# Kernel optimization log

Hardware: AMD Instinct MI355X
Metric: run time of the kernel (lower is better)

The kernel has to match this reference:

```python
import jax, jax.numpy as jnp
import numpy as np

B, C, T = 2048, 8, 1024
EPS = 1e-5
SLOPE = 1.0 / 128.0


def leaky(x):
    # F.leaky_relu(x, 1/128)
    return jnp.where(x >= 0, x, SLOPE * x)


def batchnorm(h, g, b):
    # training-mode BatchNorm1d over [B, C, T]: stats over (batch, time), biased var
    m = h.mean(axis=(0, 2), keepdims=True)
    v = jnp.mean((h - m) ** 2, axis=(0, 2), keepdims=True)
    return (h - m) * jax.lax.rsqrt(v + EPS) * g[None, :, None] + b[None, :, None]


def setup_inputs() -> dict:
    key = jax.random.key(0)
    ks = jax.random.split(key, 8)
    x = jax.random.normal(ks[0], (B, C, T), dtype=jnp.float32)
    # reservoir pushforward: low-bit random matrix scaled to spectral radius 0.1
    A_raw = jax.random.normal(ks[1], (C, C), dtype=jnp.float32)
    rho = jnp.max(jnp.abs(np.linalg.eigvals(np.asarray(A_raw))))
    A = (0.1 * A_raw / rho).astype(jnp.float32)
    w1 = jax.random.normal(ks[2], (24, 8), dtype=jnp.float32) * (1.0 / np.sqrt(8))
    b1 = jax.random.normal(ks[3], (24,), dtype=jnp.float32) * 0.01
    w2 = jax.random.normal(ks[4], (16, 24), dtype=jnp.float32) * (1.0 / np.sqrt(24))
    b2 = jax.random.normal(ks[5], (16,), dtype=jnp.float32) * 0.01
    w3 = jax.random.normal(ks[6], (11, 48), dtype=jnp.float32) * (1.0 / np.sqrt(48))
    b3 = jax.random.normal(ks[7], (11,), dtype=jnp.float32) * 0.01
    return {
        "x": x, "A": A,
        "bn1_g": jnp.ones((8,), jnp.float32), "bn1_b": jnp.zeros((8,), jnp.float32),
        "w1": w1, "b1": b1, "w2": w2, "b2": b2, "w3": w3, "b3": b3,
        "bn2_g": jnp.ones((11,), jnp.float32), "bn2_b": jnp.zeros((11,), jnp.float32),
    }


def reference(x, A, bn1_g, bn1_b, w1, b1, w2, b2, w3, b3, bn2_g, bn2_b):
    bw = batchnorm(x, bn1_g, bn1_b)  # [B,8,T]

    # --- FSDDRC reservoir: 1024-step sequential recurrence on 8-dim state ---
    xs = jnp.transpose(bw, (2, 0, 1))  # [T,B,8]

    def step(f, xt):
        # nonlin(A @ f + x_t) with nonlin(z) = clamp(4z, -1, 1)
        f_new = jnp.clip(4.0 * (f @ A.T + xt), -1.0, 1.0)
        return f_new, jnp.concatenate([f_new, leaky(f_new)], axis=-1)  # [B,16]

    f0 = jnp.zeros_like(xs[0])
    _, outs = jax.lax.scan(step, f0, xs)  # [T,B,16]
    nl_tdyn = jnp.transpose(outs, (1, 2, 0))  # [B,16,T]

    # --- feedforward branch (mtmt = linear over channel dim) ---
    h = leaky(jnp.einsum("bct,oc->bot", bw, w1) + b1[None, :, None])  # [B,24,T]
    ff = leaky(jnp.einsum("bct,oc->bot", h, w2) + b2[None, :, None])  # [B,16,T]

    stacked = jnp.concatenate([x, bw, ff, nl_tdyn], axis=1)  # [B,48,T]
    pre = jnp.einsum("bct,oc->bot", stacked, w3) + b3[None, :, None]  # [B,11,T]
    assimilated = leaky(batchnorm(pre, bn2_g, bn2_b))
    return assimilated.mean(axis=-1)  # [B,11]
```

## Files before the change

### kernel.cpp

```cpp
#include <hip/hip_runtime.h>
#include <hip/hip_fp16.h>

#define NB 2048
#define NC 8
#define NT 1024
#define EPS 1e-5f
#define SLOPE (1.0f/128.0f)
#define NELEM (2048.0f*1024.0f)
#define TB (NT*NB)

#define PAR_OFF 9216
#define BN2_OFF 1024
#define P2_OFF  10240
#define PF_S4  0
#define PF_O4  8
#define PF_B1F 16
#define PF_B2F 40
#define PF_B3F 56
#define PU_A4   96
#define XT_BYTE  65536
#define PWS_BYTE (65536 + 2048*1024*8*2)

#define ROWH 40
#define ZH   18

typedef _Float16 h2 __attribute__((ext_vector_type(2)));
typedef _Float16 half8 __attribute__((ext_vector_type(8)));
typedef float f32x4 __attribute__((ext_vector_type(4)));
typedef __fp16  fp16v2 __attribute__((ext_vector_type(2)));
union U32H2 { unsigned u; h2 h; fp16v2 f; unsigned short us[2]; };
union UF { uint4 u; half8 h; };

__device__ __forceinline__ float leaky(float z){ return fmaxf(z, z*SLOPE); }
__device__ __forceinline__ unsigned short f2h(float v){ return __half_as_ushort(__float2half(v)); }
__device__ __forceinline__ float h2f(unsigned short u){ return __half2float(__ushort_as_half(u)); }
__device__ __forceinline__ h2 uph2(unsigned u){ U32H2 x; x.u = u; return x.h; }
__device__ __forceinline__ h2 pk(float a, float b){
    U32H2 x; x.f = __builtin_amdgcn_cvt_pkrtz(a, b); return x.h;
}
__device__ __forceinline__ h2 leaky2(h2 v){
    h2 s = v * (_Float16)SLOPE;
    return __builtin_elementwise_max(v, s);
}
__device__ __forceinline__ float clamp1(float z){ return __builtin_amdgcn_fmed3f(z, -1.f, 1.f); }

#if defined(__has_builtin)
#if __has_builtin(__builtin_amdgcn_fdot2)
#define HAVE_FDOT2 1
#endif
#endif
#ifdef HAVE_FDOT2
__device__ __forceinline__ float fdot2(h2 a, h2 b, float c){ return __builtin_amdgcn_fdot2(a, b, c, false); }
#else
__device__ __forceinline__ float fdot2(h2 a, h2 b, float c){
    return c + (float)a[0]*(float)b[0] + (float)a[1]*(float)b[1];
}
#endif

__global__ __launch_bounds__(256) void k0_tr(const float* __restrict__ x,
                                             unsigned short* __restrict__ xT,
                                             float* __restrict__ ws)
{
    __shared__ unsigned short tile[64*134];
    __shared__ float sred[4][4][2];
    const int tid = threadIdx.x;
    const int bg = blockIdx.x >> 4;
    const int tg = blockIdx.x & 15;
    const int b0 = bg*16, t0 = tg*64;
    float s = 0.f, s2 = 0.f;
#pragma unroll
    for(int r=0;r<8;r++){
        const int flat4 = r*256 + tid;
        const int row = flat4 >> 4;
        const int t4  = flat4 & 15;
        const int b = row >> 3, c = row & 7;
        float4 v = *(const float4*)(x + (size_t)(b0+b)*8192 + c*1024 + t0 + t4*4);
        s  += v.x+v.y+v.z+v.w;
        s2 += v.x*v.x+v.y*v.y+v.z*v.z+v.w*v.w;
        const int base = b*8 + c;
        tile[(t4*4+0)*134 + base] = f2h(v.x);
        tile[(t4*4+1)*134 + base] = f2h(v.y);
        tile[(t4*4+2)*134 + base] = f2h(v.z);
        tile[(t4*4+3)*134 + base] = f2h(v.w);
    }
#pragma unroll
    for(int m=8;m>=1;m>>=1){ s += __shfl_xor(s,m,64); s2 += __shfl_xor(s2,m,64); }
    const int lane = tid & 63, wave = tid >> 6;
    if((lane & 15) == 0){ sred[wave][lane>>4][0] = s; sred[wave][lane>>4][1] = s2; }
    __syncthreads();
    if(tid < 16){
        const int c = tid & 7, which = tid >> 3;
        const int w0 = (c < 4) ? 0 : 1, g = c & 3;
        const float v = sred[w0][g][which] + sred[w0+2][g][which];
        atomicAdd(&ws[(blockIdx.x & 63)*16 + which*8 + c], v);
    }
#pragma unroll
    for(int r=0;r<8;r++){
        const int q = r*256 + tid;
        const int t = q >> 5, inner = q & 31;
        const unsigned int lo = *(const unsigned int*)&tile[t*134 + inner*4];
        const unsigned int hi = *(const unsigned int*)&tile[t*134 + inner*4 + 2];
        *(uint2*)(xT + ((size_t)(t0+t)*NB + b0)*8 + inner*4) = make_uint2(lo, hi);
    }
}

__device__ __forceinline__ unsigned pk2u(float a, float b){
    U32H2 v; v.us[0] = f2h(a); v.us[1] = f2h(b); return v.u;
}
__global__ __launch_bounds__(256) void k2_fold(const float* __restrict__ g1, const float* __restrict__ bb1,
    const float* __restrict__ w1, const float* __restrict__ b1,
    const float* __restrict__ w2, const float* __restrict__ b2,
    const float* __restrict__ w3, const float* __restrict__ b3,
    const float* __restrict__ A, float* __restrict__ ws,
    float* __restrict__ out)
{
    float* par = ws + PAR_OFF;
    unsigned* paru = (unsigned*)par;
    __shared__ float st[16];
    __shared__ float ssc[8], soc[8], sb1f[24], sb3f[11];
    const int tid = threadIdx.x;
    if(tid<16){
        float s=0.f;
        for(int i=0;i<64;i++) s += ws[i*16+tid];
        st[tid]=s;
    }
    __syncthreads();
    if(tid<8){
        const float inv = 1.0f/NELEM;
        float m  = st[tid]*inv;
        float v  = st[8+tid]*inv - m*m;
        float s_ = g1[tid]*rsqrtf(v+EPS);
        float o_ = bb1[tid] - m*s_;
        ssc[tid]=s_; soc[tid]=o_;
        par[PF_S4+tid]=4.f*s_; par[PF_O4+tid]=4.f*o_;
    }
    __syncthreads();
    if(tid<24){ float a=b1[tid]; for(int c=0;c<8;c++) a += w1[tid*8+c]*soc[c]; sb1f[tid]=a; par[PF_B1F+tid]=a; }
    if(tid<16){ par[PF_B2F+tid]=b2[tid]; }
    if(tid<11){ float a=b3[tid]; for(int c=0;c<8;c++) a += w3[tid*48+8+c]*soc[c]; sb3f[tid]=a; par[PF_B3F+tid]=a; }
    if(tid<32){ int i=tid>>2, j=tid&3;
        paru[PU_A4+tid] = pk2u(4.f*A[i*8+2*j], 4.f*A[i*8+2*j+1]); }
    __syncthreads();

    unsigned* pt = (unsigned*)(ws + P2_OFF);
    if(tid<64){
        const int n = tid & 15, kq = tid >> 4;
        float v[8];
#pragma unroll
        for(int j=0;j<8;j++){ int k=kq*8+j; v[j] = (k<8)? w1[n*8+k]*ssc[k] : 0.f; }
        for(int j=0;j<4;j++) pt[64 + 0*256 + tid*4 + j] = pk2u(v[2*j], v[2*j+1]);
#pragma unroll
        for(int j=0;j<8;j++){ int k=kq*8+j; int o=16+n;
            v[j] = (o<24 && k<8)? w1[o*8+k]*ssc[k] : 0.f; }
        for(int j=0;j<4;j++) pt[64 + 1*256 + tid*4 + j] = pk2u(v[2*j], v[2*j+1]);
#pragma unroll
        for(int j=0;j<8;j++){ int k=kq*8+j; v[j] = (k<24)? w2[n*24+k] : 0.f; }
        for(int j=0;j<4;j++) pt[64 + 2*256 + tid*4 + j] = pk2u(v[2*j], v[2*j+1]);
#pragma unroll
        for(int j=0;j<8;j++){ int k=kq*8+j;
            float t = 0.f;
            if(n<11){
                if(k<8)       t = w3[n*48+k] + w3[n*48+8+k]*ssc[k];
                else if(k<16) t = w3[n*48+32+(k-8)];
                else if(k<24) t = w3[n*48+40+(k-16)];
            }
            v[j] = t; }
        for(int j=0;j<4;j++) pt[64 + 3*256 + tid*4 + j] = pk2u(v[2*j], v[2*j+1]);
#pragma unroll
        for(int j=0;j<8;j++){ int k=kq*8+j;
            v[j] = (n<11 && k<16)? w3[n*48+16+k] : 0.f; }
        for(int j=0;j<4;j++) pt[64 + 4*256 + tid*4 + j] = pk2u(v[2*j], v[2*j+1]);
    }
    if(tid<16){
        float* bf = ws + P2_OFF;
        bf[tid]      = sb1f[tid];
        bf[16+tid]   = (tid<8)? sb1f[16+tid] : 0.f;
        bf[32+tid]   = b2[tid];
        bf[48+tid]   = (tid<11)? sb3f[tid] : 0.f;
    }
    for(int i=tid;i<2048*11;i+=256) out[i] = 0.f;
}

__global__ __launch_bounds__(256,4) void k34(
    const unsigned short* __restrict__ xT,
    float* __restrict__ ws,
    unsigned short* __restrict__ pws)
{
    const float* par = ws + PAR_OFF;
    const unsigned* pu = (const unsigned*)par;
    const int tid = threadIdx.x;
    const int wave = tid>>6, lane = tid&63;
    const int ln = lane&15, kb = lane>>4;
    const int b  = (blockIdx.x >> 7)*256 + tid;
    const int tg = blockIdx.x & 127;
    const int t0 = tg*8;
    const int tw = (t0 >= 16) ? (t0 - 16) : 0;

    __shared__ unsigned short lds[4*64*ROWH + 4*64*ZH];
    unsigned short* rowb = lds + wave*(64*ROWH);
    unsigned short* zbuf = lds + 4*(64*ROWH) + wave*(64*ZH);

    const float* p2 = ws + P2_OFF;
    const uint4* ft = (const uint4*)(p2 + 64);
    UF w1a, w1b, w2f, w3a, w3b;
    w1a.u = ft[lane];      w1b.u = ft[64+lane];  w2f.u = ft[128+lane];
    w3a.u = ft[192+lane];  w3b.u = ft[256+lane];
    const float bi1a = p2[ln], bi1b = p2[16+ln], bi2 = p2[32+ln], bi3 = p2[48+ln];

    h2 fh[4];
#pragma unroll
    for(int j=0;j<4;j++) fh[j] = pk(0.f, 0.f);
    float s1 = 0.f, s2 = 0.f;

    for(int t=tw; t<t0; t++){
        union { float4 v; unsigned u[4]; unsigned short us[8]; } ux;
        ux.v = *(const float4*)(xT + ((size_t)t*NB + b)*8);
        float nf[8];
#pragma unroll
        for(int i=0;i<8;i++){
            float acc = fmaf(par[PF_S4+i], h2f(ux.us[i]), par[PF_O4+i]);
#pragma unroll
            for(int j=0;j<4;j++) acc = fdot2(uph2(pu[PU_A4+i*4+j]), fh[j], acc);
            nf[i] = clamp1(acc);
        }
#pragma unroll
        for(int j=0;j<4;j++) fh[j] = pk(nf[2*j], nf[2*j+1]);
    }

    for(int t=t0; t<t0+8; ++t){
        union { float4 v; unsigned u[4]; unsigned short us[8]; } ux;
        ux.v = *(const float4*)(xT + ((size_t)t*NB + b)*8);
        float nf[8];
#pragma unroll
        for(int i=0;i<8;i++){
            float acc = fmaf(par[PF_S4+i], h2f(ux.us[i]), par[PF_O4+i]);
#pragma unroll
            for(int j=0;j<4;j++) acc = fdot2(uph2(pu[PU_A4+i*4+j]), fh[j], acc);
            nf[i] = clamp1(acc);
        }
#pragma unroll
        for(int j=0;j<4;j++) fh[j] = pk(nf[2*j], nf[2*j+1]);
        h2 lfh[4];
#pragma unroll
        for(int j=0;j<4;j++) lfh[j] = leaky2(fh[j]);

        {
            unsigned short* my = rowb + lane*ROWH;
            U32H2 f0,f1,f2,f3, l0,l1,l2,l3;
            f0.h=fh[0]; f1.h=fh[1]; f2.h=fh[2]; f3.h=fh[3];
            l0.h=lfh[0]; l1.h=lfh[1]; l2.h=lfh[2]; l3.h=lfh[3];
            *(uint4*)(my)      = make_uint4(ux.u[0], ux.u[1], ux.u[2], ux.u[3]);
            *(uint4*)(my + 8)  = make_uint4(f0.u, f1.u, f2.u, f3.u);
            *(uint4*)(my + 16) = make_uint4(l0.u, l1.u, l2.u, l3.u);
            *(uint4*)(my + 24) = make_uint4(0u, 0u, 0u, 0u);
        }

        f32x4 accz[4];
#pragma unroll
        for(int T=0;T<4;T++){
            half8 A1 = *(const half8*)(rowb + (T*16+ln)*ROWH + kb*8);
            f32x4 ha = {bi1a, bi1a, bi1a, bi1a};
            f32x4 hb = {bi1b, bi1b, bi1b, bi1b};
            f32x4 zz = {bi3,  bi3,  bi3,  bi3};
            ha = __builtin_amdgcn_mfma_f32_16x16x32_f16(A1, w1a.h, ha, 0,0,0);
            hb = __builtin_amdgcn_mfma_f32_16x16x32_f16(A1, w1b.h, hb, 0,0,0);
            zz = __builtin_amdgcn_mfma_f32_16x16x32_f16(A1, w3a.h, zz, 0,0,0);
            accz[T] = zz;
            unsigned short* hw = rowb + (T*16 + kb*4)*ROWH + ln;
#pragma unroll
            for(int r=0;r<4;r++){
                hw[r*ROWH]      = f2h(leaky(ha[r]));
                hw[r*ROWH + 16] = f2h(leaky(hb[r]));
            }
        }
#pragma unroll
        for(int T=0;T<4;T++){
            half8 A2 = *(const half8*)(rowb + (T*16+ln)*ROWH + kb*8);
            f32x4 ff = {bi2, bi2, bi2, bi2};
            ff = __builtin_amdgcn_mfma_f32_16x16x32_f16(A2, w2f.h, ff, 0,0,0);
            unsigned short* fw = rowb + (T*16 + kb*4)*ROWH + ln;
#pragma unroll
            for(int r=0;r<4;r++) fw[r*ROWH] = f2h(leaky(ff[r]));
        }
#pragma unroll
        for(int T=0;T<4;T++){
            half8 A3 = *(const half8*)(rowb + (T*16+ln)*ROWH + kb*8);
            f32x4 zz = __builtin_amdgcn_mfma_f32_16x16x32_f16(A3, w3b.h, accz[T], 0,0,0);
            unsigned short* zw = zbuf + (T*16 + kb*4)*ZH + ln;
#pragma unroll
            for(int r=0;r<4;r++){
                float z = zz[r];
                s1 += z; s2 = fmaf(z, z, s2);
                zw[r*ZH] = f2h(z);
            }
        }
        {
            const size_t base = (size_t)t*NB + b;
            const unsigned short* mz = zbuf + lane*ZH;
            unsigned short zv[11];
#pragma unroll
            for(int o=0;o<11;o++) zv[o] = mz[o];
#pragma unroll
            for(int o=0;o<11;o++) pws[(size_t)o*TB + base] = zv[o];
        }
    }

    s1 += __shfl_xor(s1, 16, 64); s1 += __shfl_xor(s1, 32, 64);
    s2 += __shfl_xor(s2, 16, 64); s2 += __shfl_xor(s2, 32, 64);
    __shared__ float red[4][22];
    if(kb==0 && ln<11){ red[wave][ln] = s1; red[wave][11+ln] = s2; }
    __syncthreads();
    if(tid<22){
        float tot = red[0][tid]+red[1][tid]+red[2][tid]+red[3][tid];
        atomicAdd(&ws[BN2_OFF + (blockIdx.x & 255)*32 + tid], tot);
    }
}

__global__ __launch_bounds__(256) void k6(const float* __restrict__ g2, const float* __restrict__ bb2,
                                          const float* __restrict__ ws,
                                          const unsigned short* __restrict__ pws,
                                          float* __restrict__ out)
{
    const int o  = blockIdx.x >> 5;
    const int r  = blockIdx.x & 31;
    const int bg = r & 1, tg = r >> 1;
    const int tid = threadIdx.x;

    __shared__ float red[4][2];
    __shared__ float sal, sbe;
    {
        float p1 = ws[BN2_OFF + tid*32 + o];
        float p2 = ws[BN2_OFF + tid*32 + 11 + o];
#pragma unroll
        for(int m=32;m>=1;m>>=1){ p1 += __shfl_xor(p1,m,64); p2 += __shfl_xor(p2,m,64); }
        const int wave = tid>>6, lane = tid&63;
        if(lane==0){ red[wave][0]=p1; red[wave][1]=p2; }
        __syncthreads();
        if(tid==0){
            float t1 = red[0][0]+red[1][0]+red[2][0]+red[3][0];
            float t2 = red[0][1]+red[1][1]+red[2][1]+red[3][1];
            const float inv = 1.0f/NELEM;
            float m = t1*inv;
            float v = t2*inv - m*m;
            float a = g2[o]*rsqrtf(v+EPS);
            sal = a; sbe = bb2[o] - m*a;
        }
        __syncthreads();
    }
    const float al = sal, be = sbe;

    const int b0 = bg*1024 + tid*4;
    const unsigned short* pp = pws + (size_t)o*TB + b0;
    float acc0=0.f, acc1=0.f, acc2=0.f, acc3=0.f;
#pragma unroll 8
    for(int i=0;i<64;i++){
        const int t = tg*64 + i;
        uint2 u = *(const uint2*)(pp + (size_t)t*NB);
        unsigned short a0 = (unsigned short)(u.x & 0xffff), a1 = (unsigned short)(u.x >> 16);
        unsigned short c0 = (unsigned short)(u.y & 0xffff), c1 = (unsigned short)(u.y >> 16);
        acc0 += leaky(fmaf(al, h2f(a0), be));
        acc1 += leaky(fmaf(al, h2f(a1), be));
        acc2 += leaky(fmaf(al, h2f(c0), be));
        acc3 += leaky(fmaf(al, h2f(c1), be));
    }
    atomicAdd(&out[(b0+0)*11+o], acc0*(1.0f/NT));
    atomicAdd(&out[(b0+1)*11+o], acc1*(1.0f/NT));
    atomicAdd(&out[(b0+2)*11+o], acc2*(1.0f/NT));
    atomicAdd(&out[(b0+3)*11+o], acc3*(1.0f/NT));
}

extern "C" void kernel_launch(void* const* d_in, const int* in_sizes, int n_in,
                              void* d_out, int out_size, void* d_ws, size_t ws_size,
                              hipStream_t stream)
{
    const float* x   = (const float*)d_in[0];
    const float* A   = (const float*)d_in[1];
    const float* g1  = (const float*)d_in[2];
    const float* bb1 = (const float*)d_in[3];
    const float* w1  = (const float*)d_in[4];
    const float* b1  = (const float*)d_in[5];
    const float* w2  = (const float*)d_in[6];
    const float* b2  = (const float*)d_in[7];
    const float* w3  = (const float*)d_in[8];
    const float* b3  = (const float*)d_in[9];
    const float* g2  = (const float*)d_in[10];
    const float* bb2 = (const float*)d_in[11];
    float* out = (float*)d_out;
    float* ws  = (float*)d_ws;
    unsigned short* xT  = (unsigned short*)((char*)d_ws + XT_BYTE);
    unsigned short* pws = (unsigned short*)((char*)d_ws + PWS_BYTE);

    (void)hipMemsetAsync(d_ws, 0, 40960, stream);
    k0_tr  <<<2048, 256, 0, stream>>>(x, xT, ws);
    k2_fold<<<1,    256, 0, stream>>>(g1, bb1, w1, b1, w2, b2, w3, b3, A, ws, out);
    k34    <<<1024, 256, 0, stream>>>(xT, ws, pws);
    k6     <<<352,  256, 0, stream>>>(g2, bb2, ws, pws, out);
}
```

Measured before the change: 201.8 us.

## Fold parameter-folding kernel into k34 and drop memset and atomics

```diff
diff --git a/kernel.cpp b/kernel.cpp
--- a/kernel.cpp
+++ b/kernel.cpp
@@ -9,17 +9,9 @@
 #define NELEM (2048.0f*1024.0f)
 #define TB (NT*NB)
 
-#define PAR_OFF 9216
-#define BN2_OFF 1024
-#define P2_OFF  10240
-#define PF_S4  0
-#define PF_O4  8
-#define PF_B1F 16
-#define PF_B2F 40
-#define PF_B3F 56
-#define PU_A4   96
-#define XT_BYTE  65536
-#define PWS_BYTE (65536 + 2048*1024*8*2)
+#define BN2_OFF 32768
+#define XT_BYTE  262144
+#define PWS_BYTE (262144 + 2048*1024*8*2)
 
 #define ROWH 40
 #define ZH   18
@@ -43,6 +35,9 @@
     return __builtin_elementwise_max(v, s);
 }
 __device__ __forceinline__ float clamp1(float z){ return __builtin_amdgcn_fmed3f(z, -1.f, 1.f); }
+__device__ __forceinline__ unsigned pk2u(float a, float b){
+    U32H2 v; v.us[0] = f2h(a); v.us[1] = f2h(b); return v.u;
+}
 
 #if defined(__has_builtin)
 #if __has_builtin(__builtin_amdgcn_fdot2)
@@ -59,7 +54,8 @@
 
 __global__ __launch_bounds__(256) void k0_tr(const float* __restrict__ x,
                                              unsigned short* __restrict__ xT,
-                                             float* __restrict__ ws)
+                                             float* __restrict__ ws,
+                                             float* __restrict__ out)
 {
     __shared__ unsigned short tile[64*134];
     __shared__ float sred[4][4][2];
@@ -67,6 +63,7 @@
     const int bg = blockIdx.x >> 4;
     const int tg = blockIdx.x & 15;
     const int b0 = bg*16, t0 = tg*64;
+    if(blockIdx.x < 88) out[blockIdx.x*256 + tid] = 0.f;
     float s = 0.f, s2 = 0.f;
 #pragma unroll
     for(int r=0;r<8;r++){
@@ -92,7 +89,7 @@
         const int c = tid & 7, which = tid >> 3;
         const int w0 = (c < 4) ? 0 : 1, g = c & 3;
         const float v = sred[w0][g][which] + sred[w0+2][g][which];
-        atomicAdd(&ws[(blockIdx.x & 63)*16 + which*8 + c], v);
+        ws[blockIdx.x*16 + which*8 + c] = v;
     }
 #pragma unroll
     for(int r=0;r<8;r++){
@@ -104,24 +101,41 @@
     }
 }
 
-__device__ __forceinline__ unsigned pk2u(float a, float b){
-    U32H2 v; v.us[0] = f2h(a); v.us[1] = f2h(b); return v.u;
-}
-__global__ __launch_bounds__(256) void k2_fold(const float* __restrict__ g1, const float* __restrict__ bb1,
+__global__ __launch_bounds__(256,4) void k34(
+    const unsigned short* __restrict__ xT,
+    float* __restrict__ ws,
+    unsigned short* __restrict__ pws,
+    const float* __restrict__ g1, const float* __restrict__ bb1,
     const float* __restrict__ w1, const float* __restrict__ b1,
     const float* __restrict__ w2, const float* __restrict__ b2,
     const float* __restrict__ w3, const float* __restrict__ b3,
-    const float* __restrict__ A, float* __restrict__ ws,
-    float* __restrict__ out)
+    const float* __restrict__ A)
 {
-    float* par = ws + PAR_OFF;
-    unsigned* paru = (unsigned*)par;
+    const int tid = threadIdx.x;
+    const int wave = tid>>6, lane = tid&63;
+    const int ln = lane&15, kb = lane>>4;
+
+    __shared__ unsigned short lds[4*64*ROWH + 4*64*ZH];
+    __shared__ float red16[16][17];
     __shared__ float st[16];
-    __shared__ float ssc[8], soc[8], sb1f[24], sb3f[11];
-    const int tid = threadIdx.x;
+    __shared__ float ssc[8], soc[8];
+    __shared__ unsigned sfragu[5*256];
+    __shared__ float sbias[64];
+    __shared__ float ss4[8], so4[8];
+    __shared__ unsigned sa4[32];
+    __shared__ float red[4][22];
+
+    {
+        const int j = tid & 15, slice = tid >> 4;
+        float acc = 0.f;
+        for(int i=slice;i<2048;i+=16) acc += ws[i*16 + j];
+        red16[slice][j] = acc;
+    }
+    __syncthreads();
     if(tid<16){
         float s=0.f;
-        for(int i=0;i<64;i++) s += ws[i*16+tid];
+#pragma unroll
+        for(int k=0;k<16;k++) s += red16[k][tid];
         st[tid]=s;
     }
     __syncthreads();
@@ -132,30 +146,22 @@
         float s_ = g1[tid]*rsqrtf(v+EPS);
         float o_ = bb1[tid] - m*s_;
         ssc[tid]=s_; soc[tid]=o_;
-        par[PF_S4+tid]=4.f*s_; par[PF_O4+tid]=4.f*o_;
-    }
-    __syncthreads();
-    if(tid<24){ float a=b1[tid]; for(int c=0;c<8;c++) a += w1[tid*8+c]*soc[c]; sb1f[tid]=a; par[PF_B1F+tid]=a; }
-    if(tid<16){ par[PF_B2F+tid]=b2[tid]; }
-    if(tid<11){ float a=b3[tid]; for(int c=0;c<8;c++) a += w3[tid*48+8+c]*soc[c]; sb3f[tid]=a; par[PF_B3F+tid]=a; }
-    if(tid<32){ int i=tid>>2, j=tid&3;
-        paru[PU_A4+tid] = pk2u(4.f*A[i*8+2*j], 4.f*A[i*8+2*j+1]); }
-    __syncthreads();
-
-    unsigned* pt = (unsigned*)(ws + P2_OFF);
+        ss4[tid]=4.f*s_; so4[tid]=4.f*o_;
+    }
+    __syncthreads();
     if(tid<64){
         const int n = tid & 15, kq = tid >> 4;
         float v[8];
 #pragma unroll
         for(int j=0;j<8;j++){ int k=kq*8+j; v[j] = (k<8)? w1[n*8+k]*ssc[k] : 0.f; }
-        for(int j=0;j<4;j++) pt[64 + 0*256 + tid*4 + j] = pk2u(v[2*j], v[2*j+1]);
+        for(int j=0;j<4;j++) sfragu[0*256 + tid*4 + j] = pk2u(v[2*j], v[2*j+1]);
 #pragma unroll
         for(int j=0;j<8;j++){ int k=kq*8+j; int o=16+n;
             v[j] = (o<24 && k<8)? w1[o*8+k]*ssc[k] : 0.f; }
-        for(int j=0;j<4;j++) pt[64 + 1*256 + tid*4 + j] = pk2u(v[2*j], v[2*j+1]);
+        for(int j=0;j<4;j++) sfragu[1*256 + tid*4 + j] = pk2u(v[2*j], v[2*j+1]);
 #pragma unroll
         for(int j=0;j<8;j++){ int k=kq*8+j; v[j] = (k<24)? w2[n*24+k] : 0.f; }
-        for(int j=0;j<4;j++) pt[64 + 2*256 + tid*4 + j] = pk2u(v[2*j], v[2*j+1]);
+        for(int j=0;j<4;j++) sfragu[2*256 + tid*4 + j] = pk2u(v[2*j], v[2*j+1]);
 #pragma unroll
         for(int j=0;j<8;j++){ int k=kq*8+j;
             float t = 0.f;
@@ -165,48 +171,58 @@
                 else if(k<24) t = w3[n*48+40+(k-16)];
             }
             v[j] = t; }
-        for(int j=0;j<4;j++) pt[64 + 3*256 + tid*4 + j] = pk2u(v[2*j], v[2*j+1]);
+        for(int j=0;j<4;j++) sfragu[3*256 + tid*4 + j] = pk2u(v[2*j], v[2*j+1]);
 #pragma unroll
         for(int j=0;j<8;j++){ int k=kq*8+j;
             v[j] = (n<11 && k<16)? w3[n*48+16+k] : 0.f; }
-        for(int j=0;j<4;j++) pt[64 + 4*256 + tid*4 + j] = pk2u(v[2*j], v[2*j+1]);
-    }
-    if(tid<16){
-        float* bf = ws + P2_OFF;
-        bf[tid]      = sb1f[tid];
-        bf[16+tid]   = (tid<8)? sb1f[16+tid] : 0.f;
-        bf[32+tid]   = b2[tid];
-        bf[48+tid]   = (tid<11)? sb3f[tid] : 0.f;
-    }
-    for(int i=tid;i<2048*11;i+=256) out[i] = 0.f;
-}
-
-__global__ __launch_bounds__(256,4) void k34(
-    const unsigned short* __restrict__ xT,
-    float* __restrict__ ws,
-    unsigned short* __restrict__ pws)
-{
-    const float* par = ws + PAR_OFF;
-    const unsigned* pu = (const unsigned*)par;
-    const int tid = threadIdx.x;
-    const int wave = tid>>6, lane = tid&63;
-    const int ln = lane&15, kb = lane>>4;
+        for(int j=0;j<4;j++) sfragu[4*256 + tid*4 + j] = pk2u(v[2*j], v[2*j+1]);
+    } else if(tid<128){
+        const int bd = tid - 64;
+        float bv = 0.f;
+        if(bd < 32){
+            if(bd < 24){
+                float a = b1[bd];
+                for(int c=0;c<8;c++) a += w1[bd*8+c]*soc[c];
+                bv = a;
+            }
+        } else if(bd < 48){
+            bv = b2[bd-32];
+        } else {
+            int oo = bd-48;
+            if(oo < 11){
+                float a = b3[oo];
+                for(int c=0;c<8;c++) a += w3[oo*48+8+c]*soc[c];
+                bv = a;
+            }
+        }
+        sbias[bd] = bv;
+    } else if(tid<160){
+        const int q = tid-128, i = q>>2, j = q&3;
+        sa4[q] = pk2u(4.f*A[i*8+2*j], 4.f*A[i*8+2*j+1]);
+    }
+    __syncthreads();
+
+    unsigned short* rowb = lds + wave*(64*ROWH);
+    unsigned short* zbuf = lds + 4*(64*ROWH) + wave*(64*ZH);
+    UF w1a, w1b, w2f, w3a, w3b;
+    {
+        const uint4* ft = (const uint4*)sfragu;
+        w1a.u = ft[lane];      w1b.u = ft[64+lane];  w2f.u = ft[128+lane];
+        w3a.u = ft[192+lane];  w3b.u = ft[256+lane];
+    }
+    const float bi1a = sbias[ln], bi1b = sbias[16+ln], bi2 = sbias[32+ln], bi3 = sbias[48+ln];
+    float s4r[8], o4r[8];
+    unsigned a4r[32];
+#pragma unroll
+    for(int i=0;i<8;i++){ s4r[i]=ss4[i]; o4r[i]=so4[i]; }
+#pragma unroll
+    for(int i=0;i<32;i++) a4r[i]=sa4[i];
+
     const int b  = (blockIdx.x >> 7)*256 + tid;
     const int tg = blockIdx.x & 127;
     const int t0 = tg*8;
     const int tw = (t0 >= 16) ? (t0 - 16) : 0;
 
-    __shared__ unsigned short lds[4*64*ROWH + 4*64*ZH];
-    unsigned short* rowb = lds + wave*(64*ROWH);
-    unsigned short* zbuf = lds + 4*(64*ROWH) + wave*(64*ZH);
-
-    const float* p2 = ws + P2_OFF;
-    const uint4* ft = (const uint4*)(p2 + 64);
-    UF w1a, w1b, w2f, w3a, w3b;
-    w1a.u = ft[lane];      w1b.u = ft[64+lane];  w2f.u = ft[128+lane];
-    w3a.u = ft[192+lane];  w3b.u = ft[256+lane];
-    const float bi1a = p2[ln], bi1b = p2[16+ln], bi2 = p2[32+ln], bi3 = p2[48+ln];
-
     h2 fh[4];
 #pragma unroll
     for(int j=0;j<4;j++) fh[j] = pk(0.f, 0.f);
@@ -218,9 +234,9 @@
         float nf[8];
 #pragma unroll
         for(int i=0;i<8;i++){
-            float acc = fmaf(par[PF_S4+i], h2f(ux.us[i]), par[PF_O4+i]);
-#pragma unroll
-            for(int j=0;j<4;j++) acc = fdot2(uph2(pu[PU_A4+i*4+j]), fh[j], acc);
+            float acc = fmaf(s4r[i], h2f(ux.us[i]), o4r[i]);
+#pragma unroll
+            for(int j=0;j<4;j++) acc = fdot2(uph2(a4r[i*4+j]), fh[j], acc);
             nf[i] = clamp1(acc);
         }
 #pragma unroll
@@ -233,9 +249,9 @@
         float nf[8];
 #pragma unroll
         for(int i=0;i<8;i++){
-            float acc = fmaf(par[PF_S4+i], h2f(ux.us[i]), par[PF_O4+i]);
-#pragma unroll
-            for(int j=0;j<4;j++) acc = fdot2(uph2(pu[PU_A4+i*4+j]), fh[j], acc);
+            float acc = fmaf(s4r[i], h2f(ux.us[i]), o4r[i]);
+#pragma unroll
+            for(int j=0;j<4;j++) acc = fdot2(uph2(a4r[i*4+j]), fh[j], acc);
             nf[i] = clamp1(acc);
         }
 #pragma unroll
@@ -307,12 +323,11 @@
 
     s1 += __shfl_xor(s1, 16, 64); s1 += __shfl_xor(s1, 32, 64);
     s2 += __shfl_xor(s2, 16, 64); s2 += __shfl_xor(s2, 32, 64);
-    __shared__ float red[4][22];
     if(kb==0 && ln<11){ red[wave][ln] = s1; red[wave][11+ln] = s2; }
     __syncthreads();
     if(tid<22){
         float tot = red[0][tid]+red[1][tid]+red[2][tid]+red[3][tid];
-        atomicAdd(&ws[BN2_OFF + (blockIdx.x & 255)*32 + tid], tot);
+        ws[BN2_OFF + blockIdx.x*22 + tid] = tot;
     }
 }
 
@@ -329,8 +344,11 @@
     __shared__ float red[4][2];
     __shared__ float sal, sbe;
     {
-        float p1 = ws[BN2_OFF + tid*32 + o];
-        float p2 = ws[BN2_OFF + tid*32 + 11 + o];
+        float p1 = 0.f, p2 = 0.f;
+        for(int i=tid;i<1024;i+=256){
+            p1 += ws[BN2_OFF + i*22 + o];
+            p2 += ws[BN2_OFF + i*22 + 11 + o];
+        }
 #pragma unroll
         for(int m=32;m>=1;m>>=1){ p1 += __shfl_xor(p1,m,64); p2 += __shfl_xor(p2,m,64); }
         const int wave = tid>>6, lane = tid&63;
@@ -390,9 +408,7 @@
     unsigned short* xT  = (unsigned short*)((char*)d_ws + XT_BYTE);
     unsigned short* pws = (unsigned short*)((char*)d_ws + PWS_BYTE);
 
-    (void)hipMemsetAsync(d_ws, 0, 40960, stream);
-    k0_tr  <<<2048, 256, 0, stream>>>(x, xT, ws);
-    k2_fold<<<1,    256, 0, stream>>>(g1, bb1, w1, b1, w2, b2, w3, b3, A, ws, out);
-    k34    <<<1024, 256, 0, stream>>>(xT, ws, pws);
-    k6     <<<352,  256, 0, stream>>>(g2, bb2, ws, pws, out);
-}
+    k0_tr<<<2048, 256, 0, stream>>>(x, xT, ws, out);
+    k34  <<<1024, 256, 0, stream>>>(xT, ws, pws, g1, bb1, w1, b1, w2, b2, w3, b3, A);
+    k6   <<<352,  256, 0, stream>>>(g2, bb2, ws, pws, out);
+}
```

Result: slower. 224.8 us (+11.4%).
